# Performance work log

Measured on AMD Instinct MI355X. Metric: run time of the kernel, lower is better.

## Reference

```python
import jax, jax.numpy as jnp
import numpy as np

B, D, H, DH, DFF = 2, 1024, 16, 64, 4096
NB, NR, S = 24, 8, 512
SCALE_DEPTH = 1.4
FSQ_DIM, FSQ_LEVELS = 32, 8
EPS = 1e-5


def rmsnorm(x, w):
    var = jnp.mean(x * x, axis=-1, keepdims=True)
    return x * jax.lax.rsqrt(var + EPS) * w


def rope_cos_sin(position):
    # position: [B] int -> cos/sin [B, DH/2]
    inv = 1.0 / (10000.0 ** (jnp.arange(0, DH, 2, dtype=jnp.float32) / DH))
    ang = position.astype(jnp.float32)[:, None] * inv[None, :]
    return jnp.cos(ang), jnp.sin(ang)


def apply_rope(x, cos, sin):
    # x: [B, H, 1, DH]
    x1, x2 = jnp.split(x, 2, axis=-1)
    c = cos[:, None, None, :]
    s = sin[:, None, None, :]
    return jnp.concatenate([x1 * c - x2 * s, x1 * s + x2 * c], axis=-1)


def run_lm(hidden, cache_k, cache_v, params, cos, sin, n_layers):
    # hidden [B,1,D]; cache_k/v [L,B,H,S,DH]; params: stacked per-layer weights.
    scale = SCALE_DEPTH / np.sqrt(n_layers)  # MuP residual scale
    inv_sqrt_dh = 1.0 / np.sqrt(DH)

    def body(h, xs):
        ln1, wq, wk, wv, wo, ln2, wg, wu, wd, ck, cv = xs
        res = h
        hn = rmsnorm(h, ln1)
        q = (hn @ wq).reshape(B, 1, H, DH).transpose(0, 2, 1, 3)
        k = (hn @ wk).reshape(B, 1, H, DH).transpose(0, 2, 1, 3)
        v = (hn @ wv).reshape(B, 1, H, DH).transpose(0, 2, 1, 3)
        q = apply_rope(q, cos, sin)
        k = apply_rope(k, cos, sin)
        nk = jnp.concatenate([ck, k], axis=2)  # [B,H,S+1,DH]
        nv = jnp.concatenate([cv, v], axis=2)
        att = jnp.einsum('bhqd,bhkd->bhqk', q, nk) * inv_sqrt_dh
        p = jax.nn.softmax(att, axis=-1)
        o = jnp.einsum('bhqk,bhkd->bhqd', p, nv).transpose(0, 2, 1, 3).reshape(B, 1, D) @ wo
        h = res + o * scale
        res = h
        hn = rmsnorm(h, ln2)
        mlp = (jax.nn.silu(hn @ wg) * (hn @ wu)) @ wd
        h = res + mlp * scale
        return h, (nk, nv)

    ln1, wq, wk, wv, wo, ln2, wg, wu, wd = params
    hidden, (nk, nv) = jax.lax.scan(
        body, hidden, (ln1, wq, wk, wv, wo, ln2, wg, wu, wd, cache_k, cache_v))
    return hidden, nk, nv


def fsq(x, w_in, w_out):
    # finite scalar quantization with straight-through rounding
    z = jnp.tanh(x @ w_in)
    half = (FSQ_LEVELS - 1) / 2.0
    zq = jnp.round(z * half) / half
    zq = z + jax.lax.stop_gradient(zq - z)
    return zq @ w_out


def _forward(position, embed, base_k, base_v, res_k, res_v,
             base_ln1, base_ln2, base_wq, base_wk, base_wv, base_wo,
             base_wg, base_wu, base_wd, base_norm,
             res_ln1, res_ln2, res_wq, res_wk, res_wv, res_wo,
             res_wg, res_wu, res_wd, res_norm,
             fsq_in, fsq_out, stop_proj_w, stop_proj_b, stop_head_w, stop_head_b):
    cos, sin = rope_cos_sin(position)
    hidden, bnk, bnv = run_lm(
        embed, base_k, base_v,
        (base_ln1, base_wq, base_wk, base_wv, base_wo, base_ln2, base_wg, base_wu, base_wd),
        cos, sin, NB)
    lm_hidden = rmsnorm(hidden, base_norm)
    lm_fsq = fsq(lm_hidden, fsq_in, fsq_out)
    stop_logit = jax.nn.silu(lm_hidden @ stop_proj_w + stop_proj_b) @ stop_head_w + stop_head_b
    res_in = lm_fsq + embed
    rh, rnk, rnv = run_lm(
        res_in, res_k, res_v,
        (res_ln1, res_wq, res_wk, res_wv, res_wo, res_ln2, res_wg, res_wu, res_wd),
        cos, sin, NR)
    rh = rmsnorm(rh, res_norm)
    return (lm_fsq, rh, stop_logit, bnk, bnv, rnk, rnv)


def setup_inputs() -> dict:
    key = jax.random.key(0)
    ks = iter(jax.random.split(key, 40))

    def p(shape, scale=0.02):
        return jax.random.normal(next(ks), shape, dtype=jnp.float32) * scale

    return {
        'embed': jax.random.normal(next(ks), (B, 1, D), jnp.float32),
        'position': jax.random.randint(next(ks), (B,), 0, S),
        'base_k': jax.random.normal(next(ks), (NB, B, H, S, DH), jnp.float32),
        'base_v': jax.random.normal(next(ks), (NB, B, H, S, DH), jnp.float32),
        'res_k': jax.random.normal(next(ks), (NR, B, H, S, DH), jnp.float32),
        'res_v': jax.random.normal(next(ks), (NR, B, H, S, DH), jnp.float32),
        'base_ln1': jnp.ones((NB, D), jnp.float32),
        'base_ln2': jnp.ones((NB, D), jnp.float32),
        'base_wq': p((NB, D, D)), 'base_wk': p((NB, D, D)),
        'base_wv': p((NB, D, D)), 'base_wo': p((NB, D, D)),
        'base_wg': p((NB, D, DFF)), 'base_wu': p((NB, D, DFF)), 'base_wd': p((NB, DFF, D)),
        'base_norm': jnp.ones((D,), jnp.float32),
        'res_ln1': jnp.ones((NR, D), jnp.float32),
        'res_ln2': jnp.ones((NR, D), jnp.float32),
        'res_wq': p((NR, D, D)), 'res_wk': p((NR, D, D)),
        'res_wv': p((NR, D, D)), 'res_wo': p((NR, D, D)),
        'res_wg': p((NR, D, DFF)), 'res_wu': p((NR, D, DFF)), 'res_wd': p((NR, DFF, D)),
        'res_norm': jnp.ones((D,), jnp.float32),
        'fsq_in': p((D, FSQ_DIM)), 'fsq_out': p((FSQ_DIM, D)),
        'stop_proj_w': p((D, D)), 'stop_proj_b': jnp.zeros((D,), jnp.float32),
        'stop_head_w': p((D, 1)), 'stop_head_b': jnp.zeros((1,), jnp.float32),
    }


def reference(embed, position, base_k, base_v, res_k, res_v,
              base_ln1, base_ln2, base_wq, base_wk, base_wv, base_wo,
              base_wg, base_wu, base_wd, base_norm,
              res_ln1, res_ln2, res_wq, res_wk, res_wv, res_wo,
              res_wg, res_wu, res_wd, res_norm,
              fsq_in, fsq_out, stop_proj_w, stop_proj_b, stop_head_w, stop_head_b):
    return _forward(position, embed, base_k, base_v, res_k, res_v,
                    base_ln1, base_ln2, base_wq, base_wk, base_wv, base_wo,
                    base_wg, base_wu, base_wd, base_norm,
                    res_ln1, res_ln2, res_wq, res_wk, res_wv, res_wo,
                    res_wg, res_wu, res_wd, res_norm,
                    fsq_in, fsq_out, stop_proj_w, stop_proj_b, stop_head_w, stop_head_b)
```

## Files before the change

### kernel.cpp

```cpp
#include <hip/hip_runtime.h>
#include <cmath>

#define D 1024
#define DFF 4096
#define NHEADS 16
#define DH 64
#define S_CACHE 512
#define SP1 513
#define NB_L 24
#define NR_L 8
#define NCH 17

#define WS_H      0
#define WS_H2     2048
#define WS_QKV    4096
#define WS_ATTN   102400
#define WS_OPROJ  139392
#define WS_GU     155776
#define WS_DOWN   286848
#define WS_SPROJ  303232

__device__ __forceinline__ float silu(float x) { return x / (1.f + expf(-x)); }

__device__ __forceinline__ void prologue_norm(
    const float* __restrict__ hbase,
    const float* __restrict__ part, int nks, float scale,
    const float* __restrict__ lnw,
    float (*hn)[D], float* __restrict__ hout)
{
  __shared__ float redw[4];
  const int t = threadIdx.x;
  const int b = t >> 7;
  const int i0 = (t & 127) * 8;
  const float4* hb4 = (const float4*)(hbase + b * D + i0);
  const float4 h0 = hb4[0], h1 = hb4[1];
  float acc[8] = {h0.x, h0.y, h0.z, h0.w, h1.x, h1.y, h1.z, h1.w};
  if (part != nullptr) {
    float s[8] = {0,0,0,0,0,0,0,0};
    for (int ks = 0; ks < nks; ++ks) {
      const float4* p4 = (const float4*)(part + (size_t)(ks * 2 + b) * D + i0);
      const float4 a = p4[0], c = p4[1];
      s[0]+=a.x; s[1]+=a.y; s[2]+=a.z; s[3]+=a.w;
      s[4]+=c.x; s[5]+=c.y; s[6]+=c.z; s[7]+=c.w;
    }
#pragma unroll
    for (int u = 0; u < 8; ++u) acc[u] += scale * s[u];
  }
  float ssq = 0.f;
#pragma unroll
  for (int u = 0; u < 8; ++u) ssq += acc[u] * acc[u];
#pragma unroll
  for (int off = 32; off; off >>= 1) ssq += __shfl_xor(ssq, off);
  if ((t & 63) == 0) redw[t >> 6] = ssq;
  __syncthreads();
  const float r = rsqrtf((redw[b * 2] + redw[b * 2 + 1]) * (1.f / D) + 1e-5f);
#pragma unroll
  for (int u = 0; u < 8; ++u) hn[b][i0 + u] = acc[u] * r * lnw[i0 + u];
  if (hout != nullptr && blockIdx.x == 0 && blockIdx.y == 0) {
    float4* o4 = (float4*)(hout + b * D + i0);
    o4[0] = make_float4(acc[0], acc[1], acc[2], acc[3]);
    o4[1] = make_float4(acc[4], acc[5], acc[6], acc[7]);
  }
  __syncthreads();
}

__global__ __launch_bounds__(256) void k_qkv(
    const float* __restrict__ hbase, const float* __restrict__ down_part,
    float* __restrict__ hout, const float* __restrict__ ln1,
    const float* __restrict__ wq, const float* __restrict__ wk,
    const float* __restrict__ wv,
    float* __restrict__ qkv_part, float scale, int has_prev)
{
  __shared__ float hn[2][D];
  __shared__ float redg[16][2][64];
  const int t = threadIdx.x;
  const int ks = blockIdx.x;
  const int cg = blockIdx.y;
  const int mat = cg >> 4;
  const int jbase = (cg & 15) * 64;
  const float* W = (mat == 0) ? wq : (mat == 1) ? wk : wv;
  const int jo4 = (t & 15) * 4;
  const int kp = t >> 4;
  const int ib = ks * 64 + kp * 4;
  float4 wbuf[4];
#pragma unroll
  for (int r = 0; r < 4; ++r)
    wbuf[r] = *(const float4*)(W + (size_t)(ib + r) * D + jbase + jo4);
  prologue_norm(hbase, has_prev ? down_part : nullptr, 8, scale, ln1, hn, hout);
  float a00=0,a01=0,a02=0,a03=0, a10=0,a11=0,a12=0,a13=0;
#pragma unroll
  for (int r = 0; r < 4; ++r) {
    const float x0 = hn[0][ib + r], x1 = hn[1][ib + r];
    a00 += wbuf[r].x*x0; a01 += wbuf[r].y*x0; a02 += wbuf[r].z*x0; a03 += wbuf[r].w*x0;
    a10 += wbuf[r].x*x1; a11 += wbuf[r].y*x1; a12 += wbuf[r].z*x1; a13 += wbuf[r].w*x1;
  }
  redg[kp][0][jo4+0]=a00; redg[kp][0][jo4+1]=a01; redg[kp][0][jo4+2]=a02; redg[kp][0][jo4+3]=a03;
  redg[kp][1][jo4+0]=a10; redg[kp][1][jo4+1]=a11; redg[kp][1][jo4+2]=a12; redg[kp][1][jo4+3]=a13;
  __syncthreads();
  if (t < 128) {
    const int b = t >> 6, jo = t & 63;
    float s = 0.f;
#pragma unroll
    for (int k2 = 0; k2 < 16; ++k2) s += redg[k2][b][jo];
    qkv_part[(size_t)((ks * 3 + mat) * 2 + b) * D + jbase + jo] = s;
  }
}

__global__ __launch_bounds__(256) void k_attn(
    const float* __restrict__ qkv_part, const int* __restrict__ position,
    const float* __restrict__ k_in, const float* __restrict__ v_in,
    float* __restrict__ k_out, float* __restrict__ v_out,
    float* __restrict__ attn_part)
{
  const int t = threadIdx.x;
  const int chunk = blockIdx.x;
  const int bh = blockIdx.y;
  const int b = bh >> 4, h = bh & 15;
  __shared__ float q[64];
  __shared__ float sc[32];
  __shared__ float red8[8][32];
  __shared__ float pvred[16][64];
  __shared__ float mlsh[2];
  __shared__ float kn[64], vn[64];
  const size_t row_in  = (size_t)bh * S_CACHE;
  const size_t row_out = (size_t)bh * SP1;
  const int pbase = (bh * NCH + chunk) * 68;

  if (chunk < 16) {
    const float4* ksrc = (const float4*)(k_in + (row_in + chunk * 32) * 64);
    float4*       kdst = (float4*)(k_out + (row_out + chunk * 32) * 64);
    const float4* vsrc = (const float4*)(v_in + (row_in + chunk * 32) * 64);
    float4*       vdst = (float4*)(v_out + (row_out + chunk * 32) * 64);
    const float4 kc0 = ksrc[t], kc1 = ksrc[t + 256];
    const float4 vc0 = vsrc[t], vc1 = vsrc[t + 256];
    kdst[t] = kc0; kdst[t + 256] = kc1;
    vdst[t] = vc0; vdst[t + 256] = vc1;
    if (t < 64) {
      float s = 0.f;
#pragma unroll
      for (int ks = 0; ks < 16; ++ks)
        s += qkv_part[(size_t)(ks * 6 + b) * D + h * 64 + t];
      q[t] = s;
    }
    __syncthreads();
    if (t < 32) {
      const float pos = (float)position[b];
      const float inv = expf(-(float)t * 0.28782313662425575f);
      const float ang = pos * inv;
      const float c = cosf(ang), sn = sinf(ang);
      const float x1 = q[t], x2 = q[t + 32];
      q[t]      = (x1 * c - x2 * sn) * 0.125f;
      q[t + 32] = (x1 * sn + x2 * c) * 0.125f;
    }
    __syncthreads();
    {
      const int key = t & 31, kp = t >> 5;
      const float* krow = k_in + (row_in + chunk * 32 + key) * 64 + kp * 8;
      const float4 k0 = *(const float4*)krow;
      const float4 k1 = *(const float4*)(krow + 4);
      const int d = kp * 8;
      float dp = k0.x*q[d] + k0.y*q[d+1] + k0.z*q[d+2] + k0.w*q[d+3]
               + k1.x*q[d+4] + k1.y*q[d+5] + k1.z*q[d+6] + k1.w*q[d+7];
      red8[kp][key] = dp;
    }
    __syncthreads();
    if (t < 32) {
      float score = 0.f;
#pragma unroll
      for (int k2 = 0; k2 < 8; ++k2) score += red8[k2][t];
      float m = score;
#pragma unroll
      for (int off = 16; off; off >>= 1) m = fmaxf(m, __shfl_xor(m, off));
      const float p = expf(score - m);
      float l = p;
#pragma unroll
      for (int off = 16; off; off >>= 1) l += __shfl_xor(l, off);
      sc[t] = p;
      if (t == 0) { mlsh[0] = m; mlsh[1] = l; }
    }
    __syncthreads();
    {
      const int d4 = (t & 15) * 4, sp = t >> 4;
      float ax = 0.f, ay = 0.f, az = 0.f, aw = 0.f;
#pragma unroll
      for (int r = 0; r < 2; ++r) {
        const int sl = sp * 2 + r;
        const float4 vv = *(const float4*)(v_in + (row_in + chunk * 32 + sl) * 64 + d4);
        const float p2 = sc[sl];
        ax += vv.x * p2; ay += vv.y * p2; az += vv.z * p2; aw += vv.w * p2;
      }
      pvred[sp][d4+0]=ax; pvred[sp][d4+1]=ay; pvred[sp][d4+2]=az; pvred[sp][d4+3]=aw;
    }
    __syncthreads();
    if (t < 64) {
      float a = 0.f;
#pragma unroll
      for (int s2 = 0; s2 < 16; ++s2) a += pvred[s2][t];
      attn_part[pbase + 2 + t] = a;
      if (t == 0) { attn_part[pbase + 0] = mlsh[0]; attn_part[pbase + 1] = mlsh[1]; }
    }
  } else {
    if (t < 64) {
      float skv = 0.f, svv = 0.f;
#pragma unroll
      for (int ks = 0; ks < 16; ++ks) {
        skv += qkv_part[(size_t)(ks * 6 + 2 + b) * D + h * 64 + t];
        svv += qkv_part[(size_t)(ks * 6 + 4 + b) * D + h * 64 + t];
      }
      kn[t] = skv; vn[t] = svv;
    }
    if (t < 64) {
      float s = 0.f;
#pragma unroll
      for (int ks = 0; ks < 16; ++ks)
        s += qkv_part[(size_t)(ks * 6 + b) * D + h * 64 + t];
      q[t] = s;
    }
    __syncthreads();
    if (t < 32) {
      const float pos = (float)position[b];
      const float inv = expf(-(float)t * 0.28782313662425575f);
      const float ang = pos * inv;
      const float c = cosf(ang), sn = sinf(ang);
      float x1 = kn[t], x2 = kn[t + 32];
      kn[t]      = x1 * c - x2 * sn;
      kn[t + 32] = x1 * sn + x2 * c;
      x1 = q[t]; x2 = q[t + 32];
      q[t]      = (x1 * c - x2 * sn) * 0.125f;
      q[t + 32] = (x1 * sn + x2 * c) * 0.125f;
    }
    __syncthreads();
    if (t < 64) {
      k_out[(row_out + S_CACHE) * 64 + t] = kn[t];
      v_out[(row_out + S_CACHE) * 64 + t] = vn[t];
      float dp = q[t] * kn[t];
#pragma unroll
      for (int off = 32; off; off >>= 1) dp += __shfl_xor(dp, off);
      attn_part[pbase + 2 + t] = vn[t];
      if (t == 0) { attn_part[pbase + 0] = dp; attn_part[pbase + 1] = 1.f; }
    }
  }
}

__global__ __launch_bounds__(256) void k_oproj(
    const float* __restrict__ attn_part, const float* __restrict__ wo,
    float* __restrict__ oproj_part)
{
  __shared__ float o[2][128];
  __shared__ float cw[2][2][NCH];
  __shared__ float redg[32][2][32];
  const int t = threadIdx.x;
  const int ks = blockIdx.x;
  const int cg = blockIdx.y;
  const int ibeg = ks * 128;
  const int jbase = cg * 32;
  const int jo4 = (t & 7) * 4;
  const int kp = t >> 3;
  float4 wbuf[4];
#pragma unroll
  for (int r = 0; r < 4; ++r)
    wbuf[r] = *(const float4*)(wo + (size_t)(ibeg + kp * 4 + r) * D + jbase + jo4);
  if (t < 4) {
    const int bb = t >> 1, hr = t & 1;
    const int hh = ks * 2 + hr;
    const int base = ((bb * 16 + hh) * NCH) * 68;
    float mg = -1e30f;
    for (int c = 0; c < NCH; ++c) mg = fmaxf(mg, attn_part[base + c * 68]);
    float lg = 0.f;
    float wloc[NCH];
    for (int c = 0; c < NCH; ++c) {
      const float w = expf(attn_part[base + c * 68] - mg);
      wloc[c] = w;
      lg += attn_part[base + c * 68 + 1] * w;
    }
    const float invl = 1.f / lg;
    for (int c = 0; c < NCH; ++c) cw[bb][hr][c] = wloc[c] * invl;
  }
  __syncthreads();
  {
    const int bb = t >> 7, ir = t & 127;
    const int i = ibeg + ir;
    const int hh = i >> 6, hr = hh - ks * 2, d = i & 63;
    float s = 0.f;
#pragma unroll
    for (int c = 0; c < NCH; ++c)
      s += attn_part[((bb * 16 + hh) * NCH + c) * 68 + 2 + d] * cw[bb][hr][c];
    o[bb][ir] = s;
  }
  __syncthreads();
  float a00=0,a01=0,a02=0,a03=0, a10=0,a11=0,a12=0,a13=0;
#pragma unroll
  for (int r = 0; r < 4; ++r) {
    const int ir = kp * 4 + r;
    const float x0 = o[0][ir], x1 = o[1][ir];
    a00 += wbuf[r].x*x0; a01 += wbuf[r].y*x0; a02 += wbuf[r].z*x0; a03 += wbuf[r].w*x0;
    a10 += wbuf[r].x*x1; a11 += wbuf[r].y*x1; a12 += wbuf[r].z*x1; a13 += wbuf[r].w*x1;
  }
  redg[kp][0][jo4+0]=a00; redg[kp][0][jo4+1]=a01; redg[kp][0][jo4+2]=a02; redg[kp][0][jo4+3]=a03;
  redg[kp][1][jo4+0]=a10; redg[kp][1][jo4+1]=a11; redg[kp][1][jo4+2]=a12; redg[kp][1][jo4+3]=a13;
  __syncthreads();
  if (t < 64) {
    const int b = t >> 5, jo = t & 31;
    float s = 0.f;
#pragma unroll
    for (int k2 = 0; k2 < 32; ++k2) s += redg[k2][b][jo];
    oproj_part[(size_t)(ks * 2 + b) * D + jbase + jo] = s;
  }
}

__global__ __launch_bounds__(256) void k_gateup(
    const float* __restrict__ hbase, const float* __restrict__ oproj_part,
    float* __restrict__ h2_out, const float* __restrict__ ln2,
    const float* __restrict__ wg, const float* __restrict__ wu,
    float* __restrict__ gu_part, float scale)
{
  __shared__ float hn[2][D];
  __shared__ float redg[16][4][64];
  const int t = threadIdx.x;
  const int ks = blockIdx.x;
  const int cg = blockIdx.y;
  const int jbase = cg * 64;
  const int jo4 = (t & 15) * 4;
  const int kp = t >> 4;
  const int ib = ks * 128 + kp * 8;
  float4 wgb[8];
#pragma unroll
  for (int r = 0; r < 8; ++r)
    wgb[r] = *(const float4*)(wg + (size_t)(ib + r) * DFF + jbase + jo4);
  prologue_norm(hbase, oproj_part, 8, scale, ln2, hn, h2_out);
  float g00=0,g01=0,g02=0,g03=0, g10=0,g11=0,g12=0,g13=0;
  float u00=0,u01=0,u02=0,u03=0, u10=0,u11=0,u12=0,u13=0;
#pragma unroll
  for (int r = 0; r < 8; ++r) {
    const float x0 = hn[0][ib + r], x1 = hn[1][ib + r];
    g00 += wgb[r].x*x0; g01 += wgb[r].y*x0; g02 += wgb[r].z*x0; g03 += wgb[r].w*x0;
    g10 += wgb[r].x*x1; g11 += wgb[r].y*x1; g12 += wgb[r].z*x1; g13 += wgb[r].w*x1;
  }
#pragma unroll
  for (int r = 0; r < 8; ++r) {
    const float4 c = *(const float4*)(wu + (size_t)(ib + r) * DFF + jbase + jo4);
    const float x0 = hn[0][ib + r], x1 = hn[1][ib + r];
    u00 += c.x*x0; u01 += c.y*x0; u02 += c.z*x0; u03 += c.w*x0;
    u10 += c.x*x1; u11 += c.y*x1; u12 += c.z*x1; u13 += c.w*x1;
  }
  redg[kp][0][jo4+0]=g00; redg[kp][0][jo4+1]=g01; redg[kp][0][jo4+2]=g02; redg[kp][0][jo4+3]=g03;
  redg[kp][1][jo4+0]=g10; redg[kp][1][jo4+1]=g11; redg[kp][1][jo4+2]=g12; redg[kp][1][jo4+3]=g13;
  redg[kp][2][jo4+0]=u00; redg[kp][2][jo4+1]=u01; redg[kp][2][jo4+2]=u02; redg[kp][2][jo4+3]=u03;
  redg[kp][3][jo4+0]=u10; redg[kp][3][jo4+1]=u11; redg[kp][3][jo4+2]=u12; redg[kp][3][jo4+3]=u13;
  __syncthreads();
  {
    const int sel = t >> 6;
    const int jo = t & 63;
    float s = 0.f;
#pragma unroll
    for (int k2 = 0; k2 < 16; ++k2) s += redg[k2][sel][jo];
    const int gm = sel >> 1, b = sel & 1;
    gu_part[(size_t)(ks * 4 + gm * 2 + b) * DFF + jbase + jo] = s;
  }
}

__global__ __launch_bounds__(256) void k_down(
    const float* __restrict__ gu_part, const float* __restrict__ wd,
    float* __restrict__ down_part)
{
  __shared__ float act[2][512];
  __shared__ float redg[32][2][32];
  const int t = threadIdx.x;
  const int ks = blockIdx.x;
  const int cg = blockIdx.y;
  const int ibeg = ks * 512;
  const int jbase = cg * 32;
  const int jo4 = (t & 7) * 4;
  const int kp = t >> 3;
  const int ib = kp * 16;
  float4 wbuf[8];
#pragma unroll
  for (int r = 0; r < 8; ++r)
    wbuf[r] = *(const float4*)(wd + (size_t)(ibeg + ib + r) * D + jbase + jo4);
#pragma unroll
  for (int u = 0; u < 4; ++u) {
    const int e = u * 256 + t;
    const int b = e >> 9, ir = e & 511;
    const int i = ibeg + ir;
    float g = 0.f, uu = 0.f;
#pragma unroll
    for (int k = 0; k < 8; ++k) {
      g  += gu_part[(size_t)(k * 4 + b) * DFF + i];
      uu += gu_part[(size_t)(k * 4 + 2 + b) * DFF + i];
    }
    act[b][ir] = silu(g) * uu;
  }
  __syncthreads();
  float a00=0,a01=0,a02=0,a03=0, a10=0,a11=0,a12=0,a13=0;
#pragma unroll
  for (int r = 0; r < 8; ++r) {
    const float x0 = act[0][ib + r], x1 = act[1][ib + r];
    a00 += wbuf[r].x*x0; a01 += wbuf[r].y*x0; a02 += wbuf[r].z*x0; a03 += wbuf[r].w*x0;
    a10 += wbuf[r].x*x1; a11 += wbuf[r].y*x1; a12 += wbuf[r].z*x1; a13 += wbuf[r].w*x1;
  }
#pragma unroll
  for (int r = 8; r < 16; ++r) {
    const float4 w = *(const float4*)(wd + (size_t)(ibeg + ib + r) * D + jbase + jo4);
    const float x0 = act[0][ib + r], x1 = act[1][ib + r];
    a00 += w.x*x0; a01 += w.y*x0; a02 += w.z*x0; a03 += w.w*x0;
    a10 += w.x*x1; a11 += w.y*x1; a12 += w.z*x1; a13 += w.w*x1;
  }
  redg[kp][0][jo4+0]=a00; redg[kp][0][jo4+1]=a01; redg[kp][0][jo4+2]=a02; redg[kp][0][jo4+3]=a03;
  redg[kp][1][jo4+0]=a10; redg[kp][1][jo4+1]=a11; redg[kp][1][jo4+2]=a12; redg[kp][1][jo4+3]=a13;
  __syncthreads();
  if (t < 64) {
    const int b = t >> 5, jo = t & 31;
    float s = 0.f;
#pragma unroll
    for (int k2 = 0; k2 < 32; ++k2) s += redg[k2][b][jo];
    down_part[(size_t)(ks * 2 + b) * D + jbase + jo] = s;
  }
}

__global__ __launch_bounds__(256) void k_heads(
    const float* __restrict__ hbase, const float* __restrict__ down_part,
    const float* __restrict__ normw, const float* __restrict__ wsp,
    float* __restrict__ sproj_part,
    const float* __restrict__ fsq_in, const float* __restrict__ fsq_out,
    const float* __restrict__ embed,
    float* __restrict__ out_fsq, float* __restrict__ h_res, float scale)
{
  __shared__ float hn[2][D];
  const int t = threadIdx.x;
  const int bid = blockIdx.x;
  if (bid < 128) {
    __shared__ float redg[16][2][64];
    const int ks = bid >> 4, cg = bid & 15;
    const int jbase = cg * 64;
    const int jo4 = (t & 15) * 4;
    const int kp = t >> 4;
    const int ib = ks * 128 + kp * 8;
    float4 wbuf[8];
#pragma unroll
    for (int r = 0; r < 8; ++r)
      wbuf[r] = *(const float4*)(wsp + (size_t)(ib + r) * D + jbase + jo4);
    prologue_norm(hbase, down_part, 8, scale, normw, hn, nullptr);
    float a00=0,a01=0,a02=0,a03=0, a10=0,a11=0,a12=0,a13=0;
#pragma unroll
    for (int r = 0; r < 8; ++r) {
      const float x0 = hn[0][ib + r], x1 = hn[1][ib + r];
      a00 += wbuf[r].x*x0; a01 += wbuf[r].y*x0; a02 += wbuf[r].z*x0; a03 += wbuf[r].w*x0;
      a10 += wbuf[r].x*x1; a11 += wbuf[r].y*x1; a12 += wbuf[r].z*x1; a13 += wbuf[r].w*x1;
    }
    redg[kp][0][jo4+0]=a00; redg[kp][0][jo4+1]=a01; redg[kp][0][jo4+2]=a02; redg[kp][0][jo4+3]=a03;
    redg[kp][1][jo4+0]=a10; redg[kp][1][jo4+1]=a11; redg[kp][1][jo4+2]=a12; redg[kp][1][jo4+3]=a13;
    __syncthreads();
    if (t < 128) {
      const int b = t >> 6, jo = t & 63;
      float s = 0.f;
#pragma unroll
      for (int k2 = 0; k2 < 16; ++k2) s += redg[k2][b][jo];
      sproj_part[(size_t)(ks * 2 + b) * D + jbase + jo] = s;
    }
  } else {
    __shared__ float zred[4][2][32];
    __shared__ float zq[2][32];
    prologue_norm(hbase, down_part, 8, scale, normw, hn, nullptr);
    {
      const int c = t & 31, b = (t >> 5) & 1, kp = t >> 6;
      float s = 0.f;
      for (int i = kp * 256; i < kp * 256 + 256; ++i) s += hn[b][i] * fsq_in[i * 32 + c];
      zred[kp][b][c] = s;
    }
    __syncthreads();
    if (t < 64) {
      const int b = t >> 5, c = t & 31;
      float z = zred[0][b][c] + zred[1][b][c] + zred[2][b][c] + zred[3][b][c];
      z = tanhf(z);
      zq[b][c] = rintf(z * 3.5f) / 3.5f;
    }
    __syncthreads();
    if (t < 128) {
      const int b = t >> 6, jo = t & 63;
      const int j = (bid - 128) * 64 + jo;
      float s = 0.f;
#pragma unroll
      for (int c = 0; c < 32; ++c) s += zq[b][c] * fsq_out[c * D + j];
      out_fsq[b * D + j] = s;
      h_res[b * D + j] = s + embed[b * D + j];
    }
  }
}

__global__ __launch_bounds__(256) void k_stophead(
    const float* __restrict__ sproj_part, const float* __restrict__ bvec,
    const float* __restrict__ hw, const float* __restrict__ hb,
    float* __restrict__ out_stop)
{
  const int t = threadIdx.x;
  float acc0 = 0.f, acc1 = 0.f;
  for (int j = t; j < D; j += 256) {
    float v0 = bvec[j], v1 = bvec[j];
#pragma unroll
    for (int ks = 0; ks < 8; ++ks) {
      v0 += sproj_part[(ks * 2 + 0) * D + j];
      v1 += sproj_part[(ks * 2 + 1) * D + j];
    }
    acc0 += silu(v0) * hw[j];
    acc1 += silu(v1) * hw[j];
  }
  __shared__ float red[256];
  red[t] = acc0;
  __syncthreads();
  for (int s = 128; s > 0; s >>= 1) { if (t < s) red[t] += red[t + s]; __syncthreads(); }
  if (t == 0) out_stop[0] = red[0] + hb[0];
  __syncthreads();
  red[t] = acc1;
  __syncthreads();
  for (int s = 128; s > 0; s >>= 1) { if (t < s) red[t] += red[t + s]; __syncthreads(); }
  if (t == 0) out_stop[1] = red[0] + hb[0];
}

__global__ __launch_bounds__(256) void k_final(
    const float* __restrict__ hbase, const float* __restrict__ down_part,
    const float* __restrict__ normw, float* __restrict__ out_rh, float scale)
{
  __shared__ float hn[2][D];
  prologue_norm(hbase, down_part, 8, scale, normw, hn, nullptr);
  const int t = threadIdx.x;
  const int b = t >> 7;
  const int i0 = (t & 127) * 8;
#pragma unroll
  for (int u = 0; u < 8; ++u) out_rh[b * D + i0 + u] = hn[b][i0 + u];
}

extern "C" void kernel_launch(void* const* d_in, const int* in_sizes, int n_in,
                              void* d_out, int out_size, void* d_ws, size_t ws_size,
                              hipStream_t stream) {
  const float* embed      = (const float*)d_in[0];
  const int*   position   = (const int*)d_in[1];
  const float* base_k     = (const float*)d_in[2];
  const float* base_v     = (const float*)d_in[3];
  const float* res_k      = (const float*)d_in[4];
  const float* res_v      = (const float*)d_in[5];
  const float* base_ln1   = (const float*)d_in[6];
  const float* base_ln2   = (const float*)d_in[7];
  const float* base_wq    = (const float*)d_in[8];
  const float* base_wk    = (const float*)d_in[9];
  const float* base_wv    = (const float*)d_in[10];
  const float* base_wo    = (const float*)d_in[11];
  const float* base_wg    = (const float*)d_in[12];
  const float* base_wu    = (const float*)d_in[13];
  const float* base_wd    = (const float*)d_in[14];
  const float* base_norm  = (const float*)d_in[15];
  const float* res_ln1    = (const float*)d_in[16];
  const float* res_ln2    = (const float*)d_in[17];
  const float* res_wq     = (const float*)d_in[18];
  const float* res_wk     = (const float*)d_in[19];
  const float* res_wv     = (const float*)d_in[20];
  const float* res_wo     = (const float*)d_in[21];
  const float* res_wg     = (const float*)d_in[22];
  const float* res_wu     = (const float*)d_in[23];
  const float* res_wd     = (const float*)d_in[24];
  const float* res_norm   = (const float*)d_in[25];
  const float* fsq_in     = (const float*)d_in[26];
  const float* fsq_out    = (const float*)d_in[27];
  const float* stop_proj_w = (const float*)d_in[28];
  const float* stop_proj_b = (const float*)d_in[29];
  const float* stop_head_w = (const float*)d_in[30];
  const float* stop_head_b = (const float*)d_in[31];

  float* out = (float*)d_out;
  float* ws = (float*)d_ws;
  float* W_h     = ws + WS_H;
  float* W_h2    = ws + WS_H2;
  float* W_qkv   = ws + WS_QKV;
  float* W_attn  = ws + WS_ATTN;
  float* W_oproj = ws + WS_OPROJ;
  float* W_gu    = ws + WS_GU;
  float* W_down  = ws + WS_DOWN;
  float* W_sproj = ws + WS_SPROJ;

  const size_t cacheL_in  = (size_t)2 * NHEADS * S_CACHE * DH;
  const size_t cacheL_out = (size_t)2 * NHEADS * SP1 * DH;
  float* out_fsq  = out;
  float* out_rh   = out + 2048;
  float* out_stop = out + 4096;
  float* out_bnk  = out + 4098;
  float* out_bnv  = out_bnk + (size_t)NB_L * cacheL_out;
  float* out_rnk  = out_bnv + (size_t)NB_L * cacheL_out;
  float* out_rnv  = out_rnk + (size_t)NR_L * cacheL_out;

  const float scaleB = 1.4f / sqrtf((float)NB_L);
  const float scaleR = 1.4f / sqrtf((float)NR_L);

  auto run_layer = [&](const float* hbase, float* hout,
                       const float* ln1, const float* ln2,
                       const float* wq, const float* wk, const float* wv,
                       const float* wo, const float* wg, const float* wu,
                       const float* wd,
                       const float* kin, const float* vin,
                       float* kout, float* vout,
                       float scale, int has_prev) {
    k_qkv<<<dim3(16, 48), 256, 0, stream>>>(hbase, W_down, hout, ln1,
                                            wq, wk, wv, W_qkv, scale, has_prev);
    k_attn<<<dim3(NCH, 32), 256, 0, stream>>>(W_qkv, position, kin, vin, kout, vout, W_attn);
    k_oproj<<<dim3(8, 32), 256, 0, stream>>>(W_attn, wo, W_oproj);
    k_gateup<<<dim3(8, 64), 256, 0, stream>>>(W_h, W_oproj, W_h2, ln2, wg, wu, W_gu, scale);
    k_down<<<dim3(8, 32), 256, 0, stream>>>(W_gu, wd, W_down);
  };

  for (int l = 0; l < NB_L; ++l) {
    run_layer(l == 0 ? embed : W_h2, W_h,
              base_ln1 + (size_t)l * D, base_ln2 + (size_t)l * D,
              base_wq + (size_t)l * D * D, base_wk + (size_t)l * D * D,
              base_wv + (size_t)l * D * D, base_wo + (size_t)l * D * D,
              base_wg + (size_t)l * D * DFF, base_wu + (size_t)l * D * DFF,
              base_wd + (size_t)l * DFF * D,
              base_k + (size_t)l * cacheL_in, base_v + (size_t)l * cacheL_in,
              out_bnk + (size_t)l * cacheL_out, out_bnv + (size_t)l * cacheL_out,
              scaleB, l > 0);
  }

  k_heads<<<144, 256, 0, stream>>>(W_h2, W_down, base_norm, stop_proj_w, W_sproj,
                                   fsq_in, fsq_out, embed, out_fsq, W_h, scaleB);
  k_stophead<<<1, 256, 0, stream>>>(W_sproj, stop_proj_b, stop_head_w, stop_head_b, out_stop);

  for (int l = 0; l < NR_L; ++l) {
    run_layer(l == 0 ? W_h : W_h2, l == 0 ? nullptr : W_h,
              res_ln1 + (size_t)l * D, res_ln2 + (size_t)l * D,
              res_wq + (size_t)l * D * D, res_wk + (size_t)l * D * D,
              res_wv + (size_t)l * D * D, res_wo + (size_t)l * D * D,
              res_wg + (size_t)l * D * DFF, res_wu + (size_t)l * D * DFF,
              res_wd + (size_t)l * DFF * D,
              res_k + (size_t)l * cacheL_in, res_v + (size_t)l * cacheL_in,
              out_rnk + (size_t)l * cacheL_out, out_rnv + (size_t)l * cacheL_out,
              scaleR, l > 0);
  }

  k_final<<<1, 256, 0, stream>>>(W_h2, W_down, res_norm, out_rh, scaleR);
}
```

Measured before the change: 1.185 ms.

## Accumulate residuals atomically and finalize RMSNorm in last block

Residual projections (o-proj and down) now atomicAdd their scaled outputs directly into a residual accumulator, and the last block to finish, tracked by a per-layer counter, computes the RMSNorm for the next stage once. The matvec kernels then read a precomputed normalized vector instead of every block re-reducing partials and redoing the norm. Attention drops the separate new-token chunk, folding it into the last chunk, and uses nontemporal stores for the KV cache copy. The down projection is split into more K-chunks. The cost is atomics and a threadfence-based last-block pattern, with float atomic summation order becoming nondeterministic.

```diff
diff --git a/kernel.cpp b/kernel.cpp
--- a/kernel.cpp
+++ b/kernel.cpp
@@ -9,69 +9,61 @@
 #define SP1 513
 #define NB_L 24
 #define NR_L 8
-#define NCH 17
-
-#define WS_H      0
-#define WS_H2     2048
-#define WS_QKV    4096
-#define WS_ATTN   102400
-#define WS_OPROJ  139392
-#define WS_GU     155776
-#define WS_DOWN   286848
-#define WS_SPROJ  303232
-
-__device__ __forceinline__ float silu(float x) { return x / (1.f + expf(-x)); }
-
-__device__ __forceinline__ void prologue_norm(
-    const float* __restrict__ hbase,
-    const float* __restrict__ part, int nks, float scale,
-    const float* __restrict__ lnw,
-    float (*hn)[D], float* __restrict__ hout)
-{
-  __shared__ float redw[4];
-  const int t = threadIdx.x;
-  const int b = t >> 7;
-  const int i0 = (t & 127) * 8;
-  const float4* hb4 = (const float4*)(hbase + b * D + i0);
-  const float4 h0 = hb4[0], h1 = hb4[1];
-  float acc[8] = {h0.x, h0.y, h0.z, h0.w, h1.x, h1.y, h1.z, h1.w};
-  if (part != nullptr) {
-    float s[8] = {0,0,0,0,0,0,0,0};
-    for (int ks = 0; ks < nks; ++ks) {
-      const float4* p4 = (const float4*)(part + (size_t)(ks * 2 + b) * D + i0);
-      const float4 a = p4[0], c = p4[1];
-      s[0]+=a.x; s[1]+=a.y; s[2]+=a.z; s[3]+=a.w;
-      s[4]+=c.x; s[5]+=c.y; s[6]+=c.z; s[7]+=c.w;
-    }
-#pragma unroll
-    for (int u = 0; u < 8; ++u) acc[u] += scale * s[u];
-  }
+#define NCH 16
+
+typedef float v4f __attribute__((ext_vector_type(4)));
+
+#define WS_HN1   0
+#define WS_HN2   2048
+#define WS_ACCO  4096
+#define WS_ACCD  6144
+#define WS_QKV   8192
+#define WS_AP    106496
+#define WS_GU    141312
+#define WS_SP    272384
+#define WS_CNT   288768
+
+__device__ __forceinline__ float silu_f(float x){ return x/(1.f+expf(-x)); }
+
+__device__ __forceinline__ void finalize_norm(
+    const float* __restrict__ acc, const float* __restrict__ normw,
+    float* __restrict__ hn_dst, float* __restrict__ acc_dst,
+    float* redw)
+{
+  const int t = threadIdx.x;
+  const int b = t >> 7, i0 = (t & 127) * 8;
+  float a[8];
+#pragma unroll
+  for (int u = 0; u < 8; ++u) a[u] = acc[b * D + i0 + u];
   float ssq = 0.f;
 #pragma unroll
-  for (int u = 0; u < 8; ++u) ssq += acc[u] * acc[u];
+  for (int u = 0; u < 8; ++u) ssq += a[u] * a[u];
 #pragma unroll
   for (int off = 32; off; off >>= 1) ssq += __shfl_xor(ssq, off);
   if ((t & 63) == 0) redw[t >> 6] = ssq;
   __syncthreads();
   const float r = rsqrtf((redw[b * 2] + redw[b * 2 + 1]) * (1.f / D) + 1e-5f);
 #pragma unroll
-  for (int u = 0; u < 8; ++u) hn[b][i0 + u] = acc[u] * r * lnw[i0 + u];
-  if (hout != nullptr && blockIdx.x == 0 && blockIdx.y == 0) {
-    float4* o4 = (float4*)(hout + b * D + i0);
-    o4[0] = make_float4(acc[0], acc[1], acc[2], acc[3]);
-    o4[1] = make_float4(acc[4], acc[5], acc[6], acc[7]);
-  }
-  __syncthreads();
+  for (int u = 0; u < 8; ++u) hn_dst[b * D + i0 + u] = a[u] * r * normw[i0 + u];
+  if (acc_dst != nullptr) {
+#pragma unroll
+    for (int u = 0; u < 8; ++u) acc_dst[b * D + i0 + u] = a[u];
+  }
+}
+
+__global__ __launch_bounds__(256) void k_init(
+    const float* __restrict__ embed, const float* __restrict__ ln1,
+    float* __restrict__ hn1, float* __restrict__ acc_o)
+{
+  __shared__ float redw[4];
+  finalize_norm(embed, ln1, hn1, acc_o, redw);
 }
 
 __global__ __launch_bounds__(256) void k_qkv(
-    const float* __restrict__ hbase, const float* __restrict__ down_part,
-    float* __restrict__ hout, const float* __restrict__ ln1,
-    const float* __restrict__ wq, const float* __restrict__ wk,
-    const float* __restrict__ wv,
-    float* __restrict__ qkv_part, float scale, int has_prev)
-{
-  __shared__ float hn[2][D];
+    const float* __restrict__ hn, const float* __restrict__ wq,
+    const float* __restrict__ wk, const float* __restrict__ wv,
+    float* __restrict__ qkv_part)
+{
   __shared__ float redg[16][2][64];
   const int t = threadIdx.x;
   const int ks = blockIdx.x;
@@ -86,13 +78,14 @@
 #pragma unroll
   for (int r = 0; r < 4; ++r)
     wbuf[r] = *(const float4*)(W + (size_t)(ib + r) * D + jbase + jo4);
-  prologue_norm(hbase, has_prev ? down_part : nullptr, 8, scale, ln1, hn, hout);
+  float x0[4], x1[4];
+#pragma unroll
+  for (int r = 0; r < 4; ++r) { x0[r] = hn[ib + r]; x1[r] = hn[D + ib + r]; }
   float a00=0,a01=0,a02=0,a03=0, a10=0,a11=0,a12=0,a13=0;
 #pragma unroll
   for (int r = 0; r < 4; ++r) {
-    const float x0 = hn[0][ib + r], x1 = hn[1][ib + r];
-    a00 += wbuf[r].x*x0; a01 += wbuf[r].y*x0; a02 += wbuf[r].z*x0; a03 += wbuf[r].w*x0;
-    a10 += wbuf[r].x*x1; a11 += wbuf[r].y*x1; a12 += wbuf[r].z*x1; a13 += wbuf[r].w*x1;
+    a00 += wbuf[r].x*x0[r]; a01 += wbuf[r].y*x0[r]; a02 += wbuf[r].z*x0[r]; a03 += wbuf[r].w*x0[r];
+    a10 += wbuf[r].x*x1[r]; a11 += wbuf[r].y*x1[r]; a12 += wbuf[r].z*x1[r]; a13 += wbuf[r].w*x1[r];
   }
   redg[kp][0][jo4+0]=a00; redg[kp][0][jo4+1]=a01; redg[kp][0][jo4+2]=a02; redg[kp][0][jo4+3]=a03;
   redg[kp][1][jo4+0]=a10; redg[kp][1][jo4+1]=a11; redg[kp][1][jo4+2]=a12; redg[kp][1][jo4+3]=a13;
@@ -116,139 +109,143 @@
   const int chunk = blockIdx.x;
   const int bh = blockIdx.y;
   const int b = bh >> 4, h = bh & 15;
-  __shared__ float q[64];
-  __shared__ float sc[32];
+  const bool hasNew = (chunk == 15);
+  __shared__ float q[64], kn[64], vn[64];
+  __shared__ float sc[33];
   __shared__ float red8[8][32];
   __shared__ float pvred[16][64];
-  __shared__ float mlsh[2];
-  __shared__ float kn[64], vn[64];
+  __shared__ float msl[3];
   const size_t row_in  = (size_t)bh * S_CACHE;
   const size_t row_out = (size_t)bh * SP1;
   const int pbase = (bh * NCH + chunk) * 68;
 
-  if (chunk < 16) {
-    const float4* ksrc = (const float4*)(k_in + (row_in + chunk * 32) * 64);
-    float4*       kdst = (float4*)(k_out + (row_out + chunk * 32) * 64);
-    const float4* vsrc = (const float4*)(v_in + (row_in + chunk * 32) * 64);
-    float4*       vdst = (float4*)(v_out + (row_out + chunk * 32) * 64);
-    const float4 kc0 = ksrc[t], kc1 = ksrc[t + 256];
-    const float4 vc0 = vsrc[t], vc1 = vsrc[t + 256];
-    kdst[t] = kc0; kdst[t + 256] = kc1;
-    vdst[t] = vc0; vdst[t + 256] = vc1;
-    if (t < 64) {
-      float s = 0.f;
-#pragma unroll
-      for (int ks = 0; ks < 16; ++ks)
-        s += qkv_part[(size_t)(ks * 6 + b) * D + h * 64 + t];
-      q[t] = s;
-    }
-    __syncthreads();
+  {
+    const v4f* ksrc = (const v4f*)(k_in + (row_in + chunk * 32) * 64);
+    const v4f* vsrc = (const v4f*)(v_in + (row_in + chunk * 32) * 64);
+    v4f* kdst = (v4f*)(k_out + (row_out + chunk * 32) * 64);
+    v4f* vdst = (v4f*)(v_out + (row_out + chunk * 32) * 64);
+    const v4f kc0 = ksrc[t], kc1 = ksrc[t + 256];
+    const v4f vc0 = vsrc[t], vc1 = vsrc[t + 256];
+    __builtin_nontemporal_store(kc0, &kdst[t]);
+    __builtin_nontemporal_store(kc1, &kdst[t + 256]);
+    __builtin_nontemporal_store(vc0, &vdst[t]);
+    __builtin_nontemporal_store(vc1, &vdst[t + 256]);
+  }
+  if (t < 64) {
+    float s = 0.f;
+#pragma unroll
+    for (int ks = 0; ks < 16; ++ks)
+      s += qkv_part[(size_t)(ks * 6 + b) * D + h * 64 + t];
+    q[t] = s;
+  } else if (hasNew && t < 128) {
+    const int u = t - 64;
+    float s = 0.f;
+#pragma unroll
+    for (int ks = 0; ks < 16; ++ks)
+      s += qkv_part[(size_t)(ks * 6 + 2 + b) * D + h * 64 + u];
+    kn[u] = s;
+  } else if (hasNew && t < 192) {
+    const int u = t - 128;
+    float s = 0.f;
+#pragma unroll
+    for (int ks = 0; ks < 16; ++ks)
+      s += qkv_part[(size_t)(ks * 6 + 4 + b) * D + h * 64 + u];
+    vn[u] = s;
+  }
+  __syncthreads();
+  {
+    const float pos = (float)position[b];
     if (t < 32) {
-      const float pos = (float)position[b];
       const float inv = expf(-(float)t * 0.28782313662425575f);
       const float ang = pos * inv;
       const float c = cosf(ang), sn = sinf(ang);
       const float x1 = q[t], x2 = q[t + 32];
       q[t]      = (x1 * c - x2 * sn) * 0.125f;
       q[t + 32] = (x1 * sn + x2 * c) * 0.125f;
-    }
-    __syncthreads();
-    {
-      const int key = t & 31, kp = t >> 5;
-      const float* krow = k_in + (row_in + chunk * 32 + key) * 64 + kp * 8;
-      const float4 k0 = *(const float4*)krow;
-      const float4 k1 = *(const float4*)(krow + 4);
-      const int d = kp * 8;
-      float dp = k0.x*q[d] + k0.y*q[d+1] + k0.z*q[d+2] + k0.w*q[d+3]
-               + k1.x*q[d+4] + k1.y*q[d+5] + k1.z*q[d+6] + k1.w*q[d+7];
-      red8[kp][key] = dp;
-    }
-    __syncthreads();
-    if (t < 32) {
-      float score = 0.f;
-#pragma unroll
-      for (int k2 = 0; k2 < 8; ++k2) score += red8[k2][t];
-      float m = score;
-#pragma unroll
-      for (int off = 16; off; off >>= 1) m = fmaxf(m, __shfl_xor(m, off));
-      const float p = expf(score - m);
-      float l = p;
-#pragma unroll
-      for (int off = 16; off; off >>= 1) l += __shfl_xor(l, off);
-      sc[t] = p;
-      if (t == 0) { mlsh[0] = m; mlsh[1] = l; }
-    }
-    __syncthreads();
-    {
-      const int d4 = (t & 15) * 4, sp = t >> 4;
-      float ax = 0.f, ay = 0.f, az = 0.f, aw = 0.f;
-#pragma unroll
-      for (int r = 0; r < 2; ++r) {
-        const int sl = sp * 2 + r;
-        const float4 vv = *(const float4*)(v_in + (row_in + chunk * 32 + sl) * 64 + d4);
-        const float p2 = sc[sl];
-        ax += vv.x * p2; ay += vv.y * p2; az += vv.z * p2; aw += vv.w * p2;
-      }
-      pvred[sp][d4+0]=ax; pvred[sp][d4+1]=ay; pvred[sp][d4+2]=az; pvred[sp][d4+3]=aw;
-    }
-    __syncthreads();
-    if (t < 64) {
-      float a = 0.f;
-#pragma unroll
-      for (int s2 = 0; s2 < 16; ++s2) a += pvred[s2][t];
-      attn_part[pbase + 2 + t] = a;
-      if (t == 0) { attn_part[pbase + 0] = mlsh[0]; attn_part[pbase + 1] = mlsh[1]; }
-    }
-  } else {
-    if (t < 64) {
-      float skv = 0.f, svv = 0.f;
-#pragma unroll
-      for (int ks = 0; ks < 16; ++ks) {
-        skv += qkv_part[(size_t)(ks * 6 + 2 + b) * D + h * 64 + t];
-        svv += qkv_part[(size_t)(ks * 6 + 4 + b) * D + h * 64 + t];
-      }
-      kn[t] = skv; vn[t] = svv;
-    }
-    if (t < 64) {
-      float s = 0.f;
-#pragma unroll
-      for (int ks = 0; ks < 16; ++ks)
-        s += qkv_part[(size_t)(ks * 6 + b) * D + h * 64 + t];
-      q[t] = s;
-    }
-    __syncthreads();
-    if (t < 32) {
-      const float pos = (float)position[b];
-      const float inv = expf(-(float)t * 0.28782313662425575f);
+    } else if (hasNew && t < 64) {
+      const int u = t - 32;
+      const float inv = expf(-(float)u * 0.28782313662425575f);
       const float ang = pos * inv;
       const float c = cosf(ang), sn = sinf(ang);
-      float x1 = kn[t], x2 = kn[t + 32];
-      kn[t]      = x1 * c - x2 * sn;
-      kn[t + 32] = x1 * sn + x2 * c;
-      x1 = q[t]; x2 = q[t + 32];
-      q[t]      = (x1 * c - x2 * sn) * 0.125f;
-      q[t + 32] = (x1 * sn + x2 * c) * 0.125f;
-    }
-    __syncthreads();
-    if (t < 64) {
-      k_out[(row_out + S_CACHE) * 64 + t] = kn[t];
-      v_out[(row_out + S_CACHE) * 64 + t] = vn[t];
-      float dp = q[t] * kn[t];
-#pragma unroll
-      for (int off = 32; off; off >>= 1) dp += __shfl_xor(dp, off);
-      attn_part[pbase + 2 + t] = vn[t];
-      if (t == 0) { attn_part[pbase + 0] = dp; attn_part[pbase + 1] = 1.f; }
-    }
+      const float x1 = kn[u], x2 = kn[u + 32];
+      kn[u]      = x1 * c - x2 * sn;
+      kn[u + 32] = x1 * sn + x2 * c;
+    }
+  }
+  __syncthreads();
+  if (hasNew && t < 64) {
+    k_out[(row_out + S_CACHE) * 64 + t] = kn[t];
+    v_out[(row_out + S_CACHE) * 64 + t] = vn[t];
+    float dp = q[t] * kn[t];
+#pragma unroll
+    for (int off = 32; off; off >>= 1) dp += __shfl_xor(dp, off);
+    if (t == 0) msl[0] = dp;
+  }
+  {
+    const int key = t & 31, kp = t >> 5;
+    const float* krow = k_in + (row_in + chunk * 32 + key) * 64 + kp * 8;
+    const float4 k0 = *(const float4*)krow;
+    const float4 k1 = *(const float4*)(krow + 4);
+    const int d = kp * 8;
+    float dp = k0.x*q[d] + k0.y*q[d+1] + k0.z*q[d+2] + k0.w*q[d+3]
+             + k1.x*q[d+4] + k1.y*q[d+5] + k1.z*q[d+6] + k1.w*q[d+7];
+    red8[kp][key] = dp;
+  }
+  __syncthreads();
+  if (t < 32) {
+    float score = 0.f;
+#pragma unroll
+    for (int k2 = 0; k2 < 8; ++k2) score += red8[k2][t];
+    float m = score;
+#pragma unroll
+    for (int off = 16; off; off >>= 1) m = fmaxf(m, __shfl_xor(m, off));
+    const float nsc = hasNew ? msl[0] : -1e30f;
+    m = fmaxf(m, nsc);
+    const float p = expf(score - m);
+    float l = p;
+#pragma unroll
+    for (int off = 16; off; off >>= 1) l += __shfl_xor(l, off);
+    sc[t] = p;
+    if (t == 0) {
+      const float pn = hasNew ? expf(nsc - m) : 0.f;
+      sc[32] = pn; msl[1] = m; msl[2] = l + pn;
+    }
+  }
+  __syncthreads();
+  {
+    const int d4 = (t & 15) * 4, sp = t >> 4;
+    float ax = 0.f, ay = 0.f, az = 0.f, aw = 0.f;
+#pragma unroll
+    for (int r = 0; r < 2; ++r) {
+      const int sl = sp * 2 + r;
+      const float4 vv = *(const float4*)(v_in + (row_in + chunk * 32 + sl) * 64 + d4);
+      const float p2 = sc[sl];
+      ax += vv.x * p2; ay += vv.y * p2; az += vv.z * p2; aw += vv.w * p2;
+    }
+    pvred[sp][d4+0]=ax; pvred[sp][d4+1]=ay; pvred[sp][d4+2]=az; pvred[sp][d4+3]=aw;
+  }
+  __syncthreads();
+  if (t < 64) {
+    float a = 0.f;
+#pragma unroll
+    for (int s2 = 0; s2 < 16; ++s2) a += pvred[s2][t];
+    if (hasNew) a += sc[32] * vn[t];
+    attn_part[pbase + 2 + t] = a;
+    if (t == 0) { attn_part[pbase + 0] = msl[1]; attn_part[pbase + 1] = msl[2]; }
   }
 }
 
 __global__ __launch_bounds__(256) void k_oproj(
     const float* __restrict__ attn_part, const float* __restrict__ wo,
-    float* __restrict__ oproj_part)
+    float* __restrict__ acc_o, float* __restrict__ acc_d,
+    float* __restrict__ hn2, const float* __restrict__ ln2,
+    int* __restrict__ cnt, float scale)
 {
   __shared__ float o[2][128];
   __shared__ float cw[2][2][NCH];
   __shared__ float redg[32][2][32];
+  __shared__ float redw[4];
+  __shared__ int s_last;
   const int t = threadIdx.x;
   const int ks = blockIdx.x;
   const int cg = blockIdx.y;
@@ -304,17 +301,25 @@
     float s = 0.f;
 #pragma unroll
     for (int k2 = 0; k2 < 32; ++k2) s += redg[k2][b][jo];
-    oproj_part[(size_t)(ks * 2 + b) * D + jbase + jo] = s;
+    atomicAdd(&acc_o[(size_t)b * D + jbase + jo], s * scale);
+  }
+  __threadfence();
+  __syncthreads();
+  if (t == 0) {
+    const int old = atomicAdd(cnt, 1);
+    s_last = (old == 8 * 32 - 1);
+  }
+  __syncthreads();
+  if (s_last) {
+    __threadfence();
+    finalize_norm(acc_o, ln2, hn2, acc_d, redw);
   }
 }
 
 __global__ __launch_bounds__(256) void k_gateup(
-    const float* __restrict__ hbase, const float* __restrict__ oproj_part,
-    float* __restrict__ h2_out, const float* __restrict__ ln2,
-    const float* __restrict__ wg, const float* __restrict__ wu,
-    float* __restrict__ gu_part, float scale)
-{
-  __shared__ float hn[2][D];
+    const float* __restrict__ hn2, const float* __restrict__ wg,
+    const float* __restrict__ wu, float* __restrict__ gu_part)
+{
   __shared__ float redg[16][4][64];
   const int t = threadIdx.x;
   const int ks = blockIdx.x;
@@ -327,21 +332,21 @@
 #pragma unroll
   for (int r = 0; r < 8; ++r)
     wgb[r] = *(const float4*)(wg + (size_t)(ib + r) * DFF + jbase + jo4);
-  prologue_norm(hbase, oproj_part, 8, scale, ln2, hn, h2_out);
+  float x0[8], x1[8];
+#pragma unroll
+  for (int r = 0; r < 8; ++r) { x0[r] = hn2[ib + r]; x1[r] = hn2[D + ib + r]; }
   float g00=0,g01=0,g02=0,g03=0, g10=0,g11=0,g12=0,g13=0;
   float u00=0,u01=0,u02=0,u03=0, u10=0,u11=0,u12=0,u13=0;
 #pragma unroll
   for (int r = 0; r < 8; ++r) {
-    const float x0 = hn[0][ib + r], x1 = hn[1][ib + r];
-    g00 += wgb[r].x*x0; g01 += wgb[r].y*x0; g02 += wgb[r].z*x0; g03 += wgb[r].w*x0;
-    g10 += wgb[r].x*x1; g11 += wgb[r].y*x1; g12 += wgb[r].z*x1; g13 += wgb[r].w*x1;
+    g00 += wgb[r].x*x0[r]; g01 += wgb[r].y*x0[r]; g02 += wgb[r].z*x0[r]; g03 += wgb[r].w*x0[r];
+    g10 += wgb[r].x*x1[r]; g11 += wgb[r].y*x1[r]; g12 += wgb[r].z*x1[r]; g13 += wgb[r].w*x1[r];
   }
 #pragma unroll
   for (int r = 0; r < 8; ++r) {
     const float4 c = *(const float4*)(wu + (size_t)(ib + r) * DFF + jbase + jo4);
-    const float x0 = hn[0][ib + r], x1 = hn[1][ib + r];
-    u00 += c.x*x0; u01 += c.y*x0; u02 += c.z*x0; u03 += c.w*x0;
-    u10 += c.x*x1; u11 += c.y*x1; u12 += c.z*x1; u13 += c.w*x1;
+    u00 += c.x*x0[r]; u01 += c.y*x0[r]; u02 += c.z*x0[r]; u03 += c.w*x0[r];
+    u10 += c.x*x1[r]; u11 += c.y*x1[r]; u12 += c.z*x1[r]; u13 += c.w*x1[r];
   }
   redg[kp][0][jo4+0]=g00; redg[kp][0][jo4+1]=g01; redg[kp][0][jo4+2]=g02; redg[kp][0][jo4+3]=g03;
   redg[kp][1][jo4+0]=g10; redg[kp][1][jo4+1]=g11; redg[kp][1][jo4+2]=g12; redg[kp][1][jo4+3]=g13;
@@ -361,26 +366,29 @@
 
 __global__ __launch_bounds__(256) void k_down(
     const float* __restrict__ gu_part, const float* __restrict__ wd,
-    float* __restrict__ down_part)
-{
-  __shared__ float act[2][512];
+    float* __restrict__ acc_d, int* __restrict__ cnt, float scale,
+    const float* __restrict__ normw, float* __restrict__ hn_dst,
+    float* __restrict__ acc_o_dst)
+{
+  __shared__ float act[2][256];
   __shared__ float redg[32][2][32];
+  __shared__ float redw[4];
+  __shared__ int s_last;
   const int t = threadIdx.x;
   const int ks = blockIdx.x;
   const int cg = blockIdx.y;
-  const int ibeg = ks * 512;
+  const int ibeg = ks * 256;
   const int jbase = cg * 32;
   const int jo4 = (t & 7) * 4;
   const int kp = t >> 3;
-  const int ib = kp * 16;
   float4 wbuf[8];
 #pragma unroll
   for (int r = 0; r < 8; ++r)
-    wbuf[r] = *(const float4*)(wd + (size_t)(ibeg + ib + r) * D + jbase + jo4);
-#pragma unroll
-  for (int u = 0; u < 4; ++u) {
+    wbuf[r] = *(const float4*)(wd + (size_t)(ibeg + kp * 8 + r) * D + jbase + jo4);
+#pragma unroll
+  for (int u = 0; u < 2; ++u) {
     const int e = u * 256 + t;
-    const int b = e >> 9, ir = e & 511;
+    const int b = e >> 8, ir = e & 255;
     const int i = ibeg + ir;
     float g = 0.f, uu = 0.f;
 #pragma unroll
@@ -388,23 +396,17 @@
       g  += gu_part[(size_t)(k * 4 + b) * DFF + i];
       uu += gu_part[(size_t)(k * 4 + 2 + b) * DFF + i];
     }
-    act[b][ir] = silu(g) * uu;
+    act[b][ir] = silu_f(g) * uu;
   }
   __syncthreads();
   float a00=0,a01=0,a02=0,a03=0, a10=0,a11=0,a12=0,a13=0;
 #pragma unroll
   for (int r = 0; r < 8; ++r) {
-    const float x0 = act[0][ib + r], x1 = act[1][ib + r];
+    const int lr = kp * 8 + r;
+    const float x0 = act[0][lr], x1 = act[1][lr];
     a00 += wbuf[r].x*x0; a01 += wbuf[r].y*x0; a02 += wbuf[r].z*x0; a03 += wbuf[r].w*x0;
     a10 += wbuf[r].x*x1; a11 += wbuf[r].y*x1; a12 += wbuf[r].z*x1; a13 += wbuf[r].w*x1;
   }
-#pragma unroll
-  for (int r = 8; r < 16; ++r) {
-    const float4 w = *(const float4*)(wd + (size_t)(ibeg + ib + r) * D + jbase + jo4);
-    const float x0 = act[0][ib + r], x1 = act[1][ib + r];
-    a00 += w.x*x0; a01 += w.y*x0; a02 += w.z*x0; a03 += w.w*x0;
-    a10 += w.x*x1; a11 += w.y*x1; a12 += w.z*x1; a13 += w.w*x1;
-  }
   redg[kp][0][jo4+0]=a00; redg[kp][0][jo4+1]=a01; redg[kp][0][jo4+2]=a02; redg[kp][0][jo4+3]=a03;
   redg[kp][1][jo4+0]=a10; redg[kp][1][jo4+1]=a11; redg[kp][1][jo4+2]=a12; redg[kp][1][jo4+3]=a13;
   __syncthreads();
@@ -413,19 +415,28 @@
     float s = 0.f;
 #pragma unroll
     for (int k2 = 0; k2 < 32; ++k2) s += redg[k2][b][jo];
-    down_part[(size_t)(ks * 2 + b) * D + jbase + jo] = s;
+    atomicAdd(&acc_d[(size_t)b * D + jbase + jo], s * scale);
+  }
+  __threadfence();
+  __syncthreads();
+  if (t == 0) {
+    const int old = atomicAdd(cnt, 1);
+    s_last = (old == 16 * 32 - 1);
+  }
+  __syncthreads();
+  if (s_last) {
+    __threadfence();
+    finalize_norm(acc_d, normw, hn_dst, acc_o_dst, redw);
   }
 }
 
 __global__ __launch_bounds__(256) void k_heads(
-    const float* __restrict__ hbase, const float* __restrict__ down_part,
-    const float* __restrict__ normw, const float* __restrict__ wsp,
+    const float* __restrict__ hn1, const float* __restrict__ wsp,
     float* __restrict__ sproj_part,
     const float* __restrict__ fsq_in, const float* __restrict__ fsq_out,
     const float* __restrict__ embed,
-    float* __restrict__ out_fsq, float* __restrict__ h_res, float scale)
-{
-  __shared__ float hn[2][D];
+    float* __restrict__ out_fsq, float* __restrict__ res_in)
+{
   const int t = threadIdx.x;
   const int bid = blockIdx.x;
   if (bid < 128) {
@@ -439,11 +450,10 @@
 #pragma unroll
     for (int r = 0; r < 8; ++r)
       wbuf[r] = *(const float4*)(wsp + (size_t)(ib + r) * D + jbase + jo4);
-    prologue_norm(hbase, down_part, 8, scale, normw, hn, nullptr);
     float a00=0,a01=0,a02=0,a03=0, a10=0,a11=0,a12=0,a13=0;
 #pragma unroll
     for (int r = 0; r < 8; ++r) {
-      const float x0 = hn[0][ib + r], x1 = hn[1][ib + r];
+      const float x0 = hn1[ib + r], x1 = hn1[D + ib + r];
       a00 += wbuf[r].x*x0; a01 += wbuf[r].y*x0; a02 += wbuf[r].z*x0; a03 += wbuf[r].w*x0;
       a10 += wbuf[r].x*x1; a11 += wbuf[r].y*x1; a12 += wbuf[r].z*x1; a13 += wbuf[r].w*x1;
     }
@@ -460,11 +470,11 @@
   } else {
     __shared__ float zred[4][2][32];
     __shared__ float zq[2][32];
-    prologue_norm(hbase, down_part, 8, scale, normw, hn, nullptr);
     {
       const int c = t & 31, b = (t >> 5) & 1, kp = t >> 6;
       float s = 0.f;
-      for (int i = kp * 256; i < kp * 256 + 256; ++i) s += hn[b][i] * fsq_in[i * 32 + c];
+      for (int i = kp * 256; i < kp * 256 + 256; ++i)
+        s += hn1[b * D + i] * fsq_in[i * 32 + c];
       zred[kp][b][c] = s;
     }
     __syncthreads();
@@ -482,7 +492,7 @@
 #pragma unroll
       for (int c = 0; c < 32; ++c) s += zq[b][c] * fsq_out[c * D + j];
       out_fsq[b * D + j] = s;
-      h_res[b * D + j] = s + embed[b * D + j];
+      res_in[b * D + j] = s + embed[b * D + j];
     }
   }
 }
@@ -490,9 +500,13 @@
 __global__ __launch_bounds__(256) void k_stophead(
     const float* __restrict__ sproj_part, const float* __restrict__ bvec,
     const float* __restrict__ hw, const float* __restrict__ hb,
-    float* __restrict__ out_stop)
-{
-  const int t = threadIdx.x;
+    float* __restrict__ out_stop,
+    const float* __restrict__ res_in, const float* __restrict__ r_ln1_0,
+    float* __restrict__ hn1, float* __restrict__ acc_o)
+{
+  const int t = threadIdx.x;
+  __shared__ float red[256];
+  __shared__ float redw[4];
   float acc0 = 0.f, acc1 = 0.f;
   for (int j = t; j < D; j += 256) {
     float v0 = bvec[j], v1 = bvec[j];
@@ -501,10 +515,9 @@
       v0 += sproj_part[(ks * 2 + 0) * D + j];
       v1 += sproj_part[(ks * 2 + 1) * D + j];
     }
-    acc0 += silu(v0) * hw[j];
-    acc1 += silu(v1) * hw[j];
-  }
-  __shared__ float red[256];
+    acc0 += silu_f(v0) * hw[j];
+    acc1 += silu_f(v1) * hw[j];
+  }
   red[t] = acc0;
   __syncthreads();
   for (int s = 128; s > 0; s >>= 1) { if (t < s) red[t] += red[t + s]; __syncthreads(); }
@@ -514,19 +527,8 @@
   __syncthreads();
   for (int s = 128; s > 0; s >>= 1) { if (t < s) red[t] += red[t + s]; __syncthreads(); }
   if (t == 0) out_stop[1] = red[0] + hb[0];
-}
-
-__global__ __launch_bounds__(256) void k_final(
-    const float* __restrict__ hbase, const float* __restrict__ down_part,
-    const float* __restrict__ normw, float* __restrict__ out_rh, float scale)
-{
-  __shared__ float hn[2][D];
-  prologue_norm(hbase, down_part, 8, scale, normw, hn, nullptr);
-  const int t = threadIdx.x;
-  const int b = t >> 7;
-  const int i0 = (t & 127) * 8;
-#pragma unroll
-  for (int u = 0; u < 8; ++u) out_rh[b * D + i0 + u] = hn[b][i0 + u];
+  __syncthreads();
+  finalize_norm(res_in, r_ln1_0, hn1, acc_o, redw);
 }
 
 extern "C" void kernel_launch(void* const* d_in, const int* in_sizes, int n_in,
@@ -566,15 +568,16 @@
   const float* stop_head_b = (const float*)d_in[31];
 
   float* out = (float*)d_out;
-  float* ws = (float*)d_ws;
-  float* W_h     = ws + WS_H;
-  float* W_h2    = ws + WS_H2;
-  float* W_qkv   = ws + WS_QKV;
-  float* W_attn  = ws + WS_ATTN;
-  float* W_oproj = ws + WS_OPROJ;
-  float* W_gu    = ws + WS_GU;
-  float* W_down  = ws + WS_DOWN;
-  float* W_sproj = ws + WS_SPROJ;
+  float* ws  = (float*)d_ws;
+  float* HN1  = ws + WS_HN1;
+  float* HN2  = ws + WS_HN2;
+  float* ACCO = ws + WS_ACCO;
+  float* ACCD = ws + WS_ACCD;
+  float* QKV  = ws + WS_QKV;
+  float* AP   = ws + WS_AP;
+  float* GU   = ws + WS_GU;
+  float* SP   = ws + WS_SP;
+  int*   CNT  = (int*)(ws + WS_CNT);
 
   const size_t cacheL_in  = (size_t)2 * NHEADS * S_CACHE * DH;
   const size_t cacheL_out = (size_t)2 * NHEADS * SP1 * DH;
@@ -589,49 +592,57 @@
   const float scaleB = 1.4f / sqrtf((float)NB_L);
   const float scaleR = 1.4f / sqrtf((float)NR_L);
 
-  auto run_layer = [&](const float* hbase, float* hout,
-                       const float* ln1, const float* ln2,
-                       const float* wq, const float* wk, const float* wv,
-                       const float* wo, const float* wg, const float* wu,
-                       const float* wd,
-                       const float* kin, const float* vin,
-                       float* kout, float* vout,
-                       float scale, int has_prev) {
-    k_qkv<<<dim3(16, 48), 256, 0, stream>>>(hbase, W_down, hout, ln1,
-                                            wq, wk, wv, W_qkv, scale, has_prev);
-    k_attn<<<dim3(NCH, 32), 256, 0, stream>>>(W_qkv, position, kin, vin, kout, vout, W_attn);
-    k_oproj<<<dim3(8, 32), 256, 0, stream>>>(W_attn, wo, W_oproj);
-    k_gateup<<<dim3(8, 64), 256, 0, stream>>>(W_h, W_oproj, W_h2, ln2, wg, wu, W_gu, scale);
-    k_down<<<dim3(8, 32), 256, 0, stream>>>(W_gu, wd, W_down);
-  };
+  (void)hipMemsetAsync(CNT, 0, 64 * sizeof(int), stream);
+  k_init<<<1, 256, 0, stream>>>(embed, base_ln1, HN1, ACCO);
 
   for (int l = 0; l < NB_L; ++l) {
-    run_layer(l == 0 ? embed : W_h2, W_h,
-              base_ln1 + (size_t)l * D, base_ln2 + (size_t)l * D,
-              base_wq + (size_t)l * D * D, base_wk + (size_t)l * D * D,
-              base_wv + (size_t)l * D * D, base_wo + (size_t)l * D * D,
-              base_wg + (size_t)l * D * DFF, base_wu + (size_t)l * D * DFF,
-              base_wd + (size_t)l * DFF * D,
-              base_k + (size_t)l * cacheL_in, base_v + (size_t)l * cacheL_in,
-              out_bnk + (size_t)l * cacheL_out, out_bnv + (size_t)l * cacheL_out,
-              scaleB, l > 0);
-  }
-
-  k_heads<<<144, 256, 0, stream>>>(W_h2, W_down, base_norm, stop_proj_w, W_sproj,
-                                   fsq_in, fsq_out, embed, out_fsq, W_h, scaleB);
-  k_stophead<<<1, 256, 0, stream>>>(W_sproj, stop_proj_b, stop_head_w, stop_head_b, out_stop);
+    const float* wq_ = base_wq + (size_t)l * D * D;
+    const float* wk_ = base_wk + (size_t)l * D * D;
+    const float* wv_ = base_wv + (size_t)l * D * D;
+    const float* wo_ = base_wo + (size_t)l * D * D;
+    const float* wg_ = base_wg + (size_t)l * D * DFF;
+    const float* wu_ = base_wu + (size_t)l * D * DFF;
+    const float* wd_ = base_wd + (size_t)l * DFF * D;
+    k_qkv<<<dim3(16, 48), 256, 0, stream>>>(HN1, wq_, wk_, wv_, QKV);
+    k_attn<<<dim3(16, 32), 256, 0, stream>>>(QKV, position,
+        base_k + (size_t)l * cacheL_in, base_v + (size_t)l * cacheL_in,
+        out_bnk + (size_t)l * cacheL_out, out_bnv + (size_t)l * cacheL_out, AP);
+    k_oproj<<<dim3(8, 32), 256, 0, stream>>>(AP, wo_, ACCO, ACCD, HN2,
+        base_ln2 + (size_t)l * D, CNT + 2 * l, scaleB);
+    k_gateup<<<dim3(8, 64), 256, 0, stream>>>(HN2, wg_, wu_, GU);
+    const float* nextw = (l + 1 < NB_L) ? (base_ln1 + (size_t)(l + 1) * D) : base_norm;
+    float* accod = (l + 1 < NB_L) ? ACCO : nullptr;
+    k_down<<<dim3(16, 32), 256, 0, stream>>>(GU, wd_, ACCD, CNT + 2 * l + 1,
+        scaleB, nextw, HN1, accod);
+  }
+
+  k_heads<<<144, 256, 0, stream>>>(HN1, stop_proj_w, SP, fsq_in, fsq_out,
+                                   embed, out_fsq, HN2);
+  k_stophead<<<1, 256, 0, stream>>>(SP, stop_proj_b, stop_head_w, stop_head_b,
+                                    out_stop, HN2, res_ln1, HN1, ACCO);
 
   for (int l = 0; l < NR_L; ++l) {
-    run_layer(l == 0 ? W_h : W_h2, l == 0 ? nullptr : W_h,
-              res_ln1 + (size_t)l * D, res_ln2 + (size_t)l * D,
-              res_wq + (size_t)l * D * D, res_wk + (size_t)l * D * D,
-              res_wv + (size_t)l * D * D, res_wo + (size_t)l * D * D,
-              res_wg + (size_t)l * D * DFF, res_wu + (size_t)l * D * DFF,
-              res_wd + (size_t)l * DFF * D,
-              res_k + (size_t)l * cacheL_in, res_v + (size_t)l * cacheL_in,
-              out_rnk + (size_t)l * cacheL_out, out_rnv + (size_t)l * cacheL_out,
-              scaleR, l > 0);
-  }
-
-  k_final<<<1, 256, 0, stream>>>(W_h2, W_down, res_norm, out_rh, scaleR);
-}
+    const int lg = NB_L + l;
+    const float* wq_ = res_wq + (size_t)l * D * D;
+    const float* wk_ = res_wk + (size_t)l * D * D;
+    const float* wv_ = res_wv + (size_t)l * D * D;
+    const float* wo_ = res_wo + (size_t)l * D * D;
+    const float* wg_ = res_wg + (size_t)l * D * DFF;
+    const float* wu_ = res_wu + (size_t)l * D * DFF;
+    const float* wd_ = res_wd + (size_t)l * DFF * D;
+    k_qkv<<<dim3(16, 48), 256, 0, stream>>>(HN1, wq_, wk_, wv_, QKV);
+    k_attn<<<dim3(16, 32), 256, 0, stream>>>(QKV, position,
+        res_k + (size_t)l * cacheL_in, res_v + (size_t)l * cacheL_in,
+        out_rnk + (size_t)l * cacheL_out, out_rnv + (size_t)l * cacheL_out, AP);
+    k_oproj<<<dim3(8, 32), 256, 0, stream>>>(AP, wo_, ACCO, ACCD, HN2,
+        res_ln2 + (size_t)l * D, CNT + 2 * lg, scaleR);
+    k_gateup<<<dim3(8, 64), 256, 0, stream>>>(HN2, wg_, wu_, GU);
+    if (l + 1 < NR_L) {
+      k_down<<<dim3(16, 32), 256, 0, stream>>>(GU, wd_, ACCD, CNT + 2 * lg + 1,
+          scaleR, res_ln1 + (size_t)(l + 1) * D, HN1, ACCO);
+    } else {
+      k_down<<<dim3(16, 32), 256, 0, stream>>>(GU, wd_, ACCD, CNT + 2 * lg + 1,
+          scaleR, res_norm, out_rh, nullptr);
+    }
+  }
+}
```

After: 3.011 ms. +154.1%, slower.
